# Performance work log

Measured on AMD Instinct MI355X. Metric: run time of the kernel, lower is better.

## Reference

```python
import jax, jax.numpy as jnp
import numpy as np

D_MODEL = 1024
N_HEADS = 16
D_HEAD = 64
BATCH = 4
SEQ = 2048
NEG = -1000000000.0


def setup_inputs() -> dict:
    key = jax.random.key(0)
    k1, k2, k3, k4, k5 = jax.random.split(key, 5)
    x = jax.random.normal(k1, (BATCH, SEQ, D_MODEL), dtype=jnp.float32)
    std = 0.02
    wq = jax.random.normal(k2, (N_HEADS, D_HEAD, D_MODEL), dtype=jnp.float32) * std
    wk = jax.random.normal(k3, (N_HEADS, D_HEAD, D_MODEL), dtype=jnp.float32) * std
    wv = jax.random.normal(k4, (N_HEADS, D_HEAD, D_MODEL), dtype=jnp.float32) * std
    wo = jax.random.normal(k5, (D_MODEL, N_HEADS * D_HEAD), dtype=jnp.float32) * std
    return {"x": x, "wq": wq, "wk": wk, "wv": wv, "wo": wo}


def reference(x, wq, wk, wv, wo):
    # x: [b, s, d_model]; wq/wk/wv: [h, d_head, d_model]; wo: [d_model, h*d_head]
    b, s, _ = x.shape
    scale = jnp.sqrt(jnp.asarray(D_HEAD, x.dtype))
    q = jnp.einsum('bsd,hed->bhse', x, wq)
    k = jnp.einsum('bsd,hed->bhse', x, wk)
    v = jnp.einsum('bsd,hed->bhse', x, wv)
    scores = jnp.einsum('bhse,bhte->bhst', q, k) / scale
    causal_mask = jnp.triu(jnp.ones((s, s), dtype=bool), k=1)
    scores = jnp.where(causal_mask, jnp.asarray(NEG, scores.dtype), scores)
    weights = jax.nn.softmax(scores, axis=-1)
    heads = jnp.einsum('bhst,bhte->bhse', weights, v)  # [b, h, s, d_head]
    concat = heads.transpose(0, 2, 1, 3).reshape(b, s, N_HEADS * D_HEAD)
    return concat @ wo.T
```

## Files before the change

kernel.cpp:

```cpp
#include <hip/hip_runtime.h>


#define DEV __device__ __forceinline__

typedef __attribute__((ext_vector_type(8))) __bf16 bf16x8;
typedef __attribute__((ext_vector_type(4))) float f32x4;
typedef unsigned short u16;

struct alignas(8) U16x4 { u16 x, y, z, w; };

DEV u16 f2bf(float f) {
  unsigned int u = __builtin_bit_cast(unsigned int, f);
  u = u + 0x7FFFu + ((u >> 16) & 1u);
  return (u16)(u >> 16);
}

DEV unsigned cvt_pk_bf16(float a, float b) {
  unsigned r;
  asm("v_cvt_pk_bf16_f32 %0, %1, %2" : "=v"(r) : "v"(a), "v"(b));
  return r;
}

DEV f32x4 mfma16(uint2 a, uint2 b, f32x4 c) {
  f32x4 d;
  asm("v_mfma_f32_16x16x16_bf16 %0, %1, %2, %3" : "=v"(d) : "v"(a), "v"(b), "v"(c));
  return d;
}

DEV void gload_lds16(const void* g, void* l) {
  __builtin_amdgcn_global_load_lds(
      (const __attribute__((address_space(1))) unsigned int*)g,
      (__attribute__((address_space(3))) unsigned int*)l, 16, 0, 0);
}

__global__ void cast_kernel(const float* __restrict__ in, u16* __restrict__ out, int n4) {
  int i = blockIdx.x * blockDim.x + threadIdx.x;
  if (i >= n4) return;
  const float4 v = reinterpret_cast<const float4*>(in)[i];
  U16x4 o{f2bf(v.x), f2bf(v.y), f2bf(v.z), f2bf(v.w)};
  reinterpret_cast<U16x4*>(out)[i] = o;
}

__global__ void cast_w_kernel(const float* __restrict__ wq, const float* __restrict__ wk,
                              const float* __restrict__ wv, const float* __restrict__ wo,
                              u16* __restrict__ wqkvb, u16* __restrict__ wob) {
  const int y = blockIdx.y;
  const int i = blockIdx.x * blockDim.x + threadIdx.x;
  const float* src = (y == 0) ? wq : (y == 1) ? wk : (y == 2) ? wv : wo;
  u16* dst = (y < 3) ? (wqkvb + (size_t)y * 1048576) : wob;
  const float4 v = reinterpret_cast<const float4*>(src)[i];
  U16x4 o{f2bf(v.x), f2bf(v.y), f2bf(v.z), f2bf(v.w)};
  reinterpret_cast<U16x4*>(dst)[i] = o;
}

template <int MODE, int NBN>
__global__ __launch_bounds__(256) void gemm_bt(
    const u16* __restrict__ A, const u16* __restrict__ B,
    void* __restrict__ C0, u16* __restrict__ vtp, int N) {
  constexpr int K = 1024;
  const int d = blockIdx.x;
  const int chunk = gridDim.x >> 3;
  const int vg = (d & 7) * chunk + (d >> 3);
  const int bn = vg % NBN, bm = vg / NBN;
  const int tid = threadIdx.x;
  const int w = tid >> 6, lane = tid & 63, lo = lane & 15, hi = lane >> 4;
  const int wm = w >> 1, wn = w & 1;

  __shared__ char lds[65536];
  char* sA = lds;
  char* sB = lds + 32768;

  const u16* Ag = A + (size_t)(bm * 128) * K;
  const u16* Bg = B + (size_t)(bn * 128) * K;

  f32x4 acc[4][4] = {};

  auto stage = [&](int buf, int k0) {
#pragma unroll
    for (int it = 0; it < 4; ++it) {
      const int L = (it * 4 + w) * 64 + lane;
      const int r = L >> 3, p = L & 7, c = p ^ (r & 7);
      gload_lds16(Ag + (size_t)r * K + k0 + c * 8, sA + buf * 16384 + (it * 4 + w) * 1024);
      gload_lds16(Bg + (size_t)r * K + k0 + c * 8, sB + buf * 16384 + (it * 4 + w) * 1024);
    }
  };

  stage(0, 0);
  __syncthreads();
  int cur = 0;
  for (int t = 0; t < 16; ++t) {
    if (t + 1 < 16) stage(cur ^ 1, (t + 1) * 64);
#pragma unroll
    for (int kc = 0; kc < 2; ++kc) {
      bf16x8 af[4], bfr[4];
#pragma unroll
      for (int m = 0; m < 4; ++m) {
        const int r = wm * 64 + m * 16 + lo;
        const int p = (kc * 4 + hi) ^ (r & 7);
        af[m] = *reinterpret_cast<const bf16x8*>(sA + cur * 16384 + r * 128 + p * 16);
      }
#pragma unroll
      for (int n = 0; n < 4; ++n) {
        const int r = wn * 64 + n * 16 + lo;
        const int p = (kc * 4 + hi) ^ (r & 7);
        bfr[n] = *reinterpret_cast<const bf16x8*>(sB + cur * 16384 + r * 128 + p * 16);
      }
#pragma unroll
      for (int m = 0; m < 4; ++m)
#pragma unroll
        for (int n = 0; n < 4; ++n)
          acc[m][n] = __builtin_amdgcn_mfma_f32_16x16x32_bf16(af[m], bfr[n], acc[m][n], 0, 0, 0);
    }
    __syncthreads();
    cur ^= 1;
  }

  const int colW = bn * 128 + wn * 64;
  const int rowW = bm * 128 + wm * 64;
  if (MODE == 0) {
    float* C = (float*)C0;
#pragma unroll
    for (int m = 0; m < 4; ++m)
#pragma unroll
      for (int n = 0; n < 4; ++n) {
        const int col = colW + n * 16 + lo;
        const int rb = rowW + m * 16 + hi * 4;
#pragma unroll
        for (int rg = 0; rg < 4; ++rg)
          C[(size_t)(rb + rg) * N + col] = acc[m][n][rg];
      }
  } else {
    u16* qkvp = (u16*)C0;
    if (bn * 128 < 2048) {
      const float qs = (bn < 8) ? 0.18033688011112042f : 1.0f;
#pragma unroll
      for (int m = 0; m < 4; ++m)
#pragma unroll
        for (int n = 0; n < 4; ++n) {
          const int col = colW + n * 16 + lo;
          const int rb = rowW + m * 16 + hi * 4;
#pragma unroll
          for (int rg = 0; rg < 4; ++rg)
            qkvp[(size_t)(rb + rg) * 2048 + col] = f2bf(acc[m][n][rg] * qs);
        }
    } else {
#pragma unroll
      for (int m = 0; m < 4; ++m)
#pragma unroll
        for (int n = 0; n < 4; ++n) {
          const int col = colW + n * 16 + lo;
          const int idx = col - 2048;
          const int hh = idx >> 6, e = idx & 63;
          const int rb = rowW + m * 16 + hi * 4;
          const int bb = rb >> 11, s = rb & 2047;
          U16x4 v4{f2bf(acc[m][n][0]), f2bf(acc[m][n][1]),
                   f2bf(acc[m][n][2]), f2bf(acc[m][n][3])};
          *reinterpret_cast<U16x4*>(vtp + ((size_t)((bb * 16 + hh) * 64 + e)) * 2048 + s) = v4;
        }
    }
  }
}

__global__ __launch_bounds__(512, 2) void attn_kernel(
    const u16* __restrict__ qkv, const u16* __restrict__ vt, u16* __restrict__ heads) {
  const int dd = blockIdx.x;
  const int vg = (dd & 7) * 32 + (dd >> 3);
  const int bx = vg & 3, bh = vg >> 2;
  const int b = bh >> 4, h = bh & 15;
  const int tid = threadIdx.x;
  const int w = tid >> 6, lane = tid & 63, lo = lane & 15, hi = lane >> 4;

  __shared__ char lds[98304];
  char* sQP = lds;
  char* sK  = lds + 32768;
  char* sV  = lds + 65536;

  const u16* Kg = qkv + (size_t)(b * 2048) * 2048 + 1024 + h * 64;
  const u16* Vg = vt + (size_t)bh * 64 * 2048;

  const int kr = tid >> 3, kc_ = (tid & 7) ^ (kr & 7);
  const int vr = tid >> 4, vc_ = (tid & 15) ^ (vr & 7);
  auto stageKV = [&](int buf, int kv0) {
#pragma unroll
    for (int it = 0; it < 2; ++it) {
      gload_lds16(Kg + (size_t)(kv0 + it * 64 + kr) * 2048 + kc_ * 8,
                  sK + buf * 16384 + it * 8192 + w * 1024);
      gload_lds16(Vg + (size_t)(it * 32 + vr) * 2048 + kv0 + vc_ * 8,
                  sV + buf * 16384 + it * 8192 + w * 1024);
    }
  };

  const int qw = w * 32;

  for (int rep = 0; rep < 2; ++rep) {
    const int qt = rep ? (7 - bx) : bx;
    const u16* Qg = qkv + (size_t)(b * 2048 + qt * 256) * 2048 + h * 64;

#pragma unroll
    for (int it = 0; it < 4; ++it) {
      const int L = it * 512 + tid;
      const int r = L >> 3, c = (L & 7) ^ (kr & 7);
      gload_lds16(Qg + (size_t)r * 2048 + c * 8, sQP + it * 8192 + w * 1024);
    }
    stageKV(0, 0);
    __syncthreads();

    bf16x8 qf[2][2];
#pragma unroll
    for (int qg = 0; qg < 2; ++qg)
#pragma unroll
      for (int kc = 0; kc < 2; ++kc) {
        const int r = qw + qg * 16 + lo;
        const int p = (kc * 4 + hi) ^ (lo & 7);
        qf[qg][kc] = *reinterpret_cast<const bf16x8*>(sQP + r * 128 + p * 16);
      }

    f32x4 lvec[2] = {};
    f32x4 oacc[2][4] = {};

    const int nt = 2 * qt + 2;
    const int qmaxw = qt * 256 + qw + 31;

    auto step = [&](int t, int cur) {
      if (t + 1 < nt) stageKV(cur ^ 1, (t + 1) * 128);
      if (t * 128 <= qmaxw) {
        f32x4 sa[2][8] = {};
        __builtin_amdgcn_s_setprio(1);
#pragma unroll
        for (int kc = 0; kc < 2; ++kc) {
#pragma unroll
          for (int n = 0; n < 8; ++n) {
            const int r = n * 16 + lo;
            const int p = (kc * 4 + hi) ^ (lo & 7);
            const bf16x8 kf = *reinterpret_cast<const bf16x8*>(sK + cur * 16384 + r * 128 + p * 16);
            sa[0][n] = __builtin_amdgcn_mfma_f32_16x16x32_bf16(kf, qf[0][kc], sa[0][n], 0, 0, 0);
            sa[1][n] = __builtin_amdgcn_mfma_f32_16x16x32_bf16(kf, qf[1][kc], sa[1][n], 0, 0, 0);
          }
        }
        __builtin_amdgcn_s_setprio(0);

        if (t >= nt - 2) {
          const int kb = t * 128 - qt * 256;
#pragma unroll
          for (int qg = 0; qg < 2; ++qg) {
            const int ql = qw + qg * 16 + lo;
#pragma unroll
            for (int n = 0; n < 8; ++n)
#pragma unroll
              for (int rg = 0; rg < 4; ++rg)
                if (kb + n * 16 + hi * 4 + rg > ql) sa[qg][n][rg] = -1e9f;
          }
        }

#pragma unroll
        for (int qg = 0; qg < 2; ++qg) {
#pragma unroll
          for (int n = 0; n < 8; ++n)
#pragma unroll
            for (int rg = 0; rg < 4; ++rg) sa[qg][n][rg] = exp2f(sa[qg][n][rg]);
          lvec[qg] += ((sa[qg][0] + sa[qg][1]) + (sa[qg][2] + sa[qg][3])) +
                      ((sa[qg][4] + sa[qg][5]) + (sa[qg][6] + sa[qg][7]));
        }

        __builtin_amdgcn_s_setprio(1);
#pragma unroll
        for (int n = 0; n < 8; ++n) {
          const uint2 pb0{cvt_pk_bf16(sa[0][n][0], sa[0][n][1]), cvt_pk_bf16(sa[0][n][2], sa[0][n][3])};
          const uint2 pb1{cvt_pk_bf16(sa[1][n][0], sa[1][n][1]), cvt_pk_bf16(sa[1][n][2], sa[1][n][3])};
          const int sb = (((2 * n + (hi >> 1)) ^ (lo & 7)) << 4) + ((hi & 1) << 3);
#pragma unroll
          for (int ne = 0; ne < 4; ++ne) {
            const uint2 vf = *reinterpret_cast<const uint2*>(
                sV + cur * 16384 + (ne * 16 + lo) * 256 + sb);
            oacc[0][ne] = mfma16(vf, pb0, oacc[0][ne]);
            oacc[1][ne] = mfma16(vf, pb1, oacc[1][ne]);
          }
        }
        __builtin_amdgcn_s_setprio(0);
      }
      __syncthreads();
    };

    for (int i = 0; i < nt; i += 2) {
      step(i, 0);
      if (i + 1 < nt) step(i + 1, 1);
    }

#pragma unroll
    for (int qg = 0; qg < 2; ++qg) {
      float lsum = (lvec[qg][0] + lvec[qg][1]) + (lvec[qg][2] + lvec[qg][3]);
      lsum += __shfl_xor(lsum, 16);
      lsum += __shfl_xor(lsum, 32);
      const float inv = 1.0f / lsum;
      const int q = qt * 256 + qw + qg * 16 + lo;
      u16* dst = heads + (size_t)(b * 2048 + q) * 1024 + h * 64;
#pragma unroll
      for (int ne = 0; ne < 4; ++ne) {
        const unsigned r0 = cvt_pk_bf16(oacc[qg][ne][0] * inv, oacc[qg][ne][1] * inv);
        const unsigned r1 = cvt_pk_bf16(oacc[qg][ne][2] * inv, oacc[qg][ne][3] * inv);
        *reinterpret_cast<uint2*>(dst + ne * 16 + hi * 4) = uint2{r0, r1};
      }
    }
  }
}

extern "C" void kernel_launch(void* const* d_in, const int* in_sizes, int n_in,
                              void* d_out, int out_size, void* d_ws, size_t ws_size,
                              hipStream_t stream) {
  const float* x  = (const float*)d_in[0];
  const float* wq = (const float*)d_in[1];
  const float* wk = (const float*)d_in[2];
  const float* wv = (const float*)d_in[3];
  const float* wo = (const float*)d_in[4];

  char* ws = (char*)d_ws;
  u16* xb    = (u16*)(ws);
  u16* wqkvb = (u16*)(ws + 16777216);
  u16* wob   = (u16*)(ws + 23068672);
  u16* qkv   = (u16*)(ws + 25165824);
  u16* vtp   = (u16*)(ws + 58720256);
  u16* heads = (u16*)(ws + 75497472);

  cast_kernel<<<8192, 256, 0, stream>>>(x, xb, 2097152);
  cast_w_kernel<<<dim3(1024, 4), 256, 0, stream>>>(wq, wk, wv, wo, wqkvb, wob);

  gemm_bt<1, 24><<<1536, 256, 0, stream>>>(xb, wqkvb, qkv, vtp, 3072);
  attn_kernel<<<256, 512, 0, stream>>>(qkv, vtp, heads);
  gemm_bt<0, 8><<<512, 256, 0, stream>>>(heads, wob, d_out, nullptr, 1024);
}
```

Baseline: 179.4 us.

## Split attention into one query tile per block with smaller KV tiles

The attention kernel now gives each block a single 256-row query tile instead of a balanced pair, so the grid doubles to 512 blocks, heaviest-first. KV tiles shrink from 128 to 64 keys, which cuts LDS from 96KB to 64KB and the launch-bounds occupancy hint rises from 2 to 4 blocks. The aim is better occupancy and latency hiding. In exchange, per-block work is uneven and there are twice as many barriers per key processed.

```diff
diff --git a/kernel.cpp b/kernel.cpp
--- a/kernel.cpp
+++ b/kernel.cpp
@@ -161,145 +161,139 @@
   }
 }
 
-__global__ __launch_bounds__(512, 2) void attn_kernel(
+__global__ __launch_bounds__(512, 4) void attn_kernel(
     const u16* __restrict__ qkv, const u16* __restrict__ vt, u16* __restrict__ heads) {
   const int dd = blockIdx.x;
-  const int vg = (dd & 7) * 32 + (dd >> 3);
-  const int bx = vg & 3, bh = vg >> 2;
+  const int x = dd & 7, k = dd >> 3;
+  const int bh = x + 8 * (k & 7);
+  const int bx = 7 - (k >> 3);
   const int b = bh >> 4, h = bh & 15;
   const int tid = threadIdx.x;
   const int w = tid >> 6, lane = tid & 63, lo = lane & 15, hi = lane >> 4;
 
-  __shared__ char lds[98304];
-  char* sQP = lds;
-  char* sK  = lds + 32768;
-  char* sV  = lds + 65536;
-
+  __shared__ char lds[65536];
+  char* sQ = lds;
+  char* sK = lds + 32768;
+  char* sV = lds + 49152;
+
+  const int qbase = bx * 256;
+  const u16* Qg = qkv + (size_t)(b * 2048 + qbase) * 2048 + h * 64;
   const u16* Kg = qkv + (size_t)(b * 2048) * 2048 + 1024 + h * 64;
   const u16* Vg = vt + (size_t)bh * 64 * 2048;
 
-  const int kr = tid >> 3, kc_ = (tid & 7) ^ (kr & 7);
-  const int vr = tid >> 4, vc_ = (tid & 15) ^ (vr & 7);
-  auto stageKV = [&](int buf, int kv0) {
-#pragma unroll
-    for (int it = 0; it < 2; ++it) {
-      gload_lds16(Kg + (size_t)(kv0 + it * 64 + kr) * 2048 + kc_ * 8,
-                  sK + buf * 16384 + it * 8192 + w * 1024);
-      gload_lds16(Vg + (size_t)(it * 32 + vr) * 2048 + kv0 + vc_ * 8,
-                  sV + buf * 16384 + it * 8192 + w * 1024);
-    }
+  const int r64 = tid >> 3, c8 = (tid & 7) ^ (r64 & 7);
+#pragma unroll
+  for (int it = 0; it < 4; ++it) {
+    const int r = it * 64 + r64;
+    gload_lds16(Qg + (size_t)r * 2048 + c8 * 8, sQ + it * 8192 + w * 1024);
+  }
+  const u16* Kst = Kg + (size_t)r64 * 2048 + c8 * 8;
+  const u16* Vst = Vg + (size_t)r64 * 2048 + c8 * 8;
+  gload_lds16(Kst, sK + w * 1024);
+  gload_lds16(Vst, sV + w * 1024);
+  Kst += (size_t)64 * 2048;
+  Vst += 64;
+  __syncthreads();
+
+  const int qw = w * 32;
+  bf16x8 qf[2][2];
+#pragma unroll
+  for (int qg = 0; qg < 2; ++qg)
+#pragma unroll
+    for (int kc = 0; kc < 2; ++kc) {
+      const int r = qw + qg * 16 + lo;
+      const int p = (kc * 4 + hi) ^ (lo & 7);
+      qf[qg][kc] = *reinterpret_cast<const bf16x8*>(sQ + r * 128 + p * 16);
+    }
+
+  f32x4 lvec[2] = {};
+  f32x4 oacc[2][4] = {};
+
+  const int nt = (bx + 1) * 4;
+  const int qmaxw = qbase + qw + 31;
+
+  auto step = [&](int t, int cur) {
+    if (t + 1 < nt) {
+      gload_lds16(Kst, sK + (cur ^ 1) * 8192 + w * 1024);
+      gload_lds16(Vst, sV + (cur ^ 1) * 8192 + w * 1024);
+      Kst += (size_t)64 * 2048;
+      Vst += 64;
+    }
+    if (t * 64 <= qmaxw) {
+      f32x4 sa[2][4] = {};
+      __builtin_amdgcn_s_setprio(1);
+#pragma unroll
+      for (int kc = 0; kc < 2; ++kc) {
+#pragma unroll
+        for (int n = 0; n < 4; ++n) {
+          const int r = n * 16 + lo;
+          const int p = (kc * 4 + hi) ^ (lo & 7);
+          const bf16x8 kf = *reinterpret_cast<const bf16x8*>(sK + cur * 8192 + r * 128 + p * 16);
+          sa[0][n] = __builtin_amdgcn_mfma_f32_16x16x32_bf16(kf, qf[0][kc], sa[0][n], 0, 0, 0);
+          sa[1][n] = __builtin_amdgcn_mfma_f32_16x16x32_bf16(kf, qf[1][kc], sa[1][n], 0, 0, 0);
+        }
+      }
+      __builtin_amdgcn_s_setprio(0);
+
+      if (t >= nt - 4) {
+        const int kb = t * 64 - qbase;
+#pragma unroll
+        for (int qg = 0; qg < 2; ++qg) {
+          const int thr = qw + qg * 16 + lo - kb;
+#pragma unroll
+          for (int n = 0; n < 4; ++n)
+#pragma unroll
+            for (int rg = 0; rg < 4; ++rg)
+              if (n * 16 + hi * 4 + rg > thr) sa[qg][n][rg] = -1e9f;
+        }
+      }
+
+#pragma unroll
+      for (int qg = 0; qg < 2; ++qg) {
+#pragma unroll
+        for (int n = 0; n < 4; ++n)
+#pragma unroll
+          for (int rg = 0; rg < 4; ++rg) sa[qg][n][rg] = exp2f(sa[qg][n][rg]);
+        lvec[qg] += (sa[qg][0] + sa[qg][1]) + (sa[qg][2] + sa[qg][3]);
+      }
+
+      __builtin_amdgcn_s_setprio(1);
+#pragma unroll
+      for (int n = 0; n < 4; ++n) {
+        const uint2 pb0{cvt_pk_bf16(sa[0][n][0], sa[0][n][1]), cvt_pk_bf16(sa[0][n][2], sa[0][n][3])};
+        const uint2 pb1{cvt_pk_bf16(sa[1][n][0], sa[1][n][1]), cvt_pk_bf16(sa[1][n][2], sa[1][n][3])};
+        const int sb = (((2 * n + (hi >> 1)) ^ (lo & 7)) << 4) + ((hi & 1) << 3);
+#pragma unroll
+        for (int ne = 0; ne < 4; ++ne) {
+          const uint2 vf = *reinterpret_cast<const uint2*>(
+              sV + cur * 8192 + (ne * 16 + lo) * 128 + sb);
+          oacc[0][ne] = mfma16(vf, pb0, oacc[0][ne]);
+          oacc[1][ne] = mfma16(vf, pb1, oacc[1][ne]);
+        }
+      }
+      __builtin_amdgcn_s_setprio(0);
+    }
+    __syncthreads();
   };
 
-  const int qw = w * 32;
-
-  for (int rep = 0; rep < 2; ++rep) {
-    const int qt = rep ? (7 - bx) : bx;
-    const u16* Qg = qkv + (size_t)(b * 2048 + qt * 256) * 2048 + h * 64;
-
-#pragma unroll
-    for (int it = 0; it < 4; ++it) {
-      const int L = it * 512 + tid;
-      const int r = L >> 3, c = (L & 7) ^ (kr & 7);
-      gload_lds16(Qg + (size_t)r * 2048 + c * 8, sQP + it * 8192 + w * 1024);
-    }
-    stageKV(0, 0);
-    __syncthreads();
-
-    bf16x8 qf[2][2];
-#pragma unroll
-    for (int qg = 0; qg < 2; ++qg)
-#pragma unroll
-      for (int kc = 0; kc < 2; ++kc) {
-        const int r = qw + qg * 16 + lo;
-        const int p = (kc * 4 + hi) ^ (lo & 7);
-        qf[qg][kc] = *reinterpret_cast<const bf16x8*>(sQP + r * 128 + p * 16);
-      }
-
-    f32x4 lvec[2] = {};
-    f32x4 oacc[2][4] = {};
-
-    const int nt = 2 * qt + 2;
-    const int qmaxw = qt * 256 + qw + 31;
-
-    auto step = [&](int t, int cur) {
-      if (t + 1 < nt) stageKV(cur ^ 1, (t + 1) * 128);
-      if (t * 128 <= qmaxw) {
-        f32x4 sa[2][8] = {};
-        __builtin_amdgcn_s_setprio(1);
-#pragma unroll
-        for (int kc = 0; kc < 2; ++kc) {
-#pragma unroll
-          for (int n = 0; n < 8; ++n) {
-            const int r = n * 16 + lo;
-            const int p = (kc * 4 + hi) ^ (lo & 7);
-            const bf16x8 kf = *reinterpret_cast<const bf16x8*>(sK + cur * 16384 + r * 128 + p * 16);
-            sa[0][n] = __builtin_amdgcn_mfma_f32_16x16x32_bf16(kf, qf[0][kc], sa[0][n], 0, 0, 0);
-            sa[1][n] = __builtin_amdgcn_mfma_f32_16x16x32_bf16(kf, qf[1][kc], sa[1][n], 0, 0, 0);
-          }
-        }
-        __builtin_amdgcn_s_setprio(0);
-
-        if (t >= nt - 2) {
-          const int kb = t * 128 - qt * 256;
-#pragma unroll
-          for (int qg = 0; qg < 2; ++qg) {
-            const int ql = qw + qg * 16 + lo;
-#pragma unroll
-            for (int n = 0; n < 8; ++n)
-#pragma unroll
-              for (int rg = 0; rg < 4; ++rg)
-                if (kb + n * 16 + hi * 4 + rg > ql) sa[qg][n][rg] = -1e9f;
-          }
-        }
-
-#pragma unroll
-        for (int qg = 0; qg < 2; ++qg) {
-#pragma unroll
-          for (int n = 0; n < 8; ++n)
-#pragma unroll
-            for (int rg = 0; rg < 4; ++rg) sa[qg][n][rg] = exp2f(sa[qg][n][rg]);
-          lvec[qg] += ((sa[qg][0] + sa[qg][1]) + (sa[qg][2] + sa[qg][3])) +
-                      ((sa[qg][4] + sa[qg][5]) + (sa[qg][6] + sa[qg][7]));
-        }
-
-        __builtin_amdgcn_s_setprio(1);
-#pragma unroll
-        for (int n = 0; n < 8; ++n) {
-          const uint2 pb0{cvt_pk_bf16(sa[0][n][0], sa[0][n][1]), cvt_pk_bf16(sa[0][n][2], sa[0][n][3])};
-          const uint2 pb1{cvt_pk_bf16(sa[1][n][0], sa[1][n][1]), cvt_pk_bf16(sa[1][n][2], sa[1][n][3])};
-          const int sb = (((2 * n + (hi >> 1)) ^ (lo & 7)) << 4) + ((hi & 1) << 3);
-#pragma unroll
-          for (int ne = 0; ne < 4; ++ne) {
-            const uint2 vf = *reinterpret_cast<const uint2*>(
-                sV + cur * 16384 + (ne * 16 + lo) * 256 + sb);
-            oacc[0][ne] = mfma16(vf, pb0, oacc[0][ne]);
-            oacc[1][ne] = mfma16(vf, pb1, oacc[1][ne]);
-          }
-        }
-        __builtin_amdgcn_s_setprio(0);
-      }
-      __syncthreads();
-    };
-
-    for (int i = 0; i < nt; i += 2) {
-      step(i, 0);
-      if (i + 1 < nt) step(i + 1, 1);
-    }
-
-#pragma unroll
-    for (int qg = 0; qg < 2; ++qg) {
-      float lsum = (lvec[qg][0] + lvec[qg][1]) + (lvec[qg][2] + lvec[qg][3]);
-      lsum += __shfl_xor(lsum, 16);
-      lsum += __shfl_xor(lsum, 32);
-      const float inv = 1.0f / lsum;
-      const int q = qt * 256 + qw + qg * 16 + lo;
-      u16* dst = heads + (size_t)(b * 2048 + q) * 1024 + h * 64;
-#pragma unroll
-      for (int ne = 0; ne < 4; ++ne) {
-        const unsigned r0 = cvt_pk_bf16(oacc[qg][ne][0] * inv, oacc[qg][ne][1] * inv);
-        const unsigned r1 = cvt_pk_bf16(oacc[qg][ne][2] * inv, oacc[qg][ne][3] * inv);
-        *reinterpret_cast<uint2*>(dst + ne * 16 + hi * 4) = uint2{r0, r1};
-      }
+  for (int i = 0; i < nt; i += 2) {
+    step(i, 0);
+    step(i + 1, 1);
+  }
+
+#pragma unroll
+  for (int qg = 0; qg < 2; ++qg) {
+    float lsum = (lvec[qg][0] + lvec[qg][1]) + (lvec[qg][2] + lvec[qg][3]);
+    lsum += __shfl_xor(lsum, 16);
+    lsum += __shfl_xor(lsum, 32);
+    const float inv = 1.0f / lsum;
+    const int q = qbase + qw + qg * 16 + lo;
+    u16* dst = heads + (size_t)(b * 2048 + q) * 1024 + h * 64;
+#pragma unroll
+    for (int ne = 0; ne < 4; ++ne) {
+      const unsigned r0 = cvt_pk_bf16(oacc[qg][ne][0] * inv, oacc[qg][ne][1] * inv);
+      const unsigned r1 = cvt_pk_bf16(oacc[qg][ne][2] * inv, oacc[qg][ne][3] * inv);
+      *reinterpret_cast<uint2*>(dst + ne * 16 + hi * 4) = uint2{r0, r1};
     }
   }
 }
@@ -325,6 +319,6 @@
   cast_w_kernel<<<dim3(1024, 4), 256, 0, stream>>>(wq, wk, wv, wo, wqkvb, wob);
 
   gemm_bt<1, 24><<<1536, 256, 0, stream>>>(xb, wqkvb, qkv, vtp, 3072);
-  attn_kernel<<<256, 512, 0, stream>>>(qkv, vtp, heads);
+  attn_kernel<<<512, 512, 0, stream>>>(qkv, vtp, heads);
   gemm_bt<0, 8><<<512, 256, 0, stream>>>(heads, wob, d_out, nullptr, 1024);
 }
```

After: 184.9 us. 3.1% more time.
